# Kernel tuning notes

Measured on AMD Instinct MI355X. Metric: run time of the kernel, lower is better.

The kernel has to match this reference:

```python
import jax, jax.numpy as jnp
import numpy as np

B, C_IN, L = 1024, 3, 2048
D, K = 64, 8192          # embedding_dim, num_embeddings
BETA = 0.25
SLOPE = 0.001            # LeakyReLU negative slope


def _leaky(x):
    return jnp.where(x > 0, x, SLOPE * x)


def setup_inputs() -> dict:
    key = jax.random.key(0)
    ks = jax.random.split(key, 16)
    def lin(k, fan_in, shape):  # torch default conv init ~ U(-1/sqrt(fan_in), 1/sqrt(fan_in))
        b = 1.0 / np.sqrt(fan_in)
        return jax.random.uniform(k, shape, jnp.float32, -b, b)
    inp = {
        "x":  jax.random.normal(ks[0], (B, C_IN, L), jnp.float32),
        # encoder conv1x1 weights stored as [out, in]
        "W1": lin(ks[1], C_IN, (64, C_IN)),  "b1": lin(ks[2], C_IN, (64,)),
        "W2": lin(ks[3], 64,   (128, 64)),   "b2": lin(ks[4], 64,  (128,)),
        "W3": lin(ks[5], 128,  (D, 128)),    "b3": lin(ks[6], 128, (D,)),
        # codebook init: uniform(-1/K, 1/K) as in the torch module
        "codebook": jax.random.uniform(ks[7], (K, D), jnp.float32, -1.0 / K, 1.0 / K),
        # decoder convtranspose1x1 weights stored as [in, out]
        "U1": lin(ks[8],  D,   (D, 128)),    "c1": lin(ks[9],  D,   (128,)),
        "U2": lin(ks[10], 128, (128, 64)),   "c2": lin(ks[11], 128, (64,)),
        "U3": lin(ks[12], 64,  (64, C_IN)),  "c3": lin(ks[13], 64,  (C_IN,)),
    }
    return inp


def reference(x, W1, b1, W2, b2, W3, b3, codebook, U1, c1, U2, c2, U3, c3):
    # ---- encoder: conv1x1 stack over [B, C, L] then global max pool ----
    h = _leaky(jnp.einsum('oc,bcl->bol', W1, x) + b1[None, :, None])   # [B,64,L]
    h = _leaky(jnp.einsum('oc,bcl->bol', W2, h) + b2[None, :, None])   # [B,128,L]
    h = jnp.einsum('oc,bcl->bol', W3, h) + b3[None, :, None]           # [B,D,L]
    z = jnp.max(h, axis=-1)                                            # [B,D]

    # ---- vector quantizer ----
    d = (jnp.sum(z * z, axis=1, keepdims=True)
         + jnp.sum(codebook * codebook, axis=1)
         - 2.0 * z @ codebook.T)                                       # [B,K]
    idx = jnp.argmin(d, axis=1)                                        # [B]
    z_q = codebook[idx]                                                # [B,D]
    sg = jax.lax.stop_gradient
    loss = jnp.mean((sg(z_q) - z) ** 2) + BETA * jnp.mean((z_q - sg(z)) ** 2)
    z_q_st = z + sg(z_q - z)                                           # straight-through

    # ---- decoder: convtranspose1x1 on length-1 sequence == dense layers ----
    g = _leaky(z_q_st @ U1 + c1)                                       # [B,128]
    g = _leaky(g @ U2 + c2)                                            # [B,64]
    x_recon = (g @ U3 + c3)[:, :, None]                                # [B,3,1]
    return x_recon, loss, z
```

## Files before the change

### kernel.cpp

```cpp
#include <hip/hip_runtime.h>
#include <hip/hip_bf16.h>

#define BB 1024
#define LL 2048
#define KK 8192

typedef _Float16 f16x8 __attribute__((ext_vector_type(8)));
typedef _Float16 f16x4 __attribute__((ext_vector_type(4)));
typedef _Float16 f16x2 __attribute__((ext_vector_type(2)));
typedef float    f32x4 __attribute__((ext_vector_type(4)));

__device__ __forceinline__ float leakyf(float v){ return fmaxf(v, 0.001f*v); }
__device__ __forceinline__ f16x2 pkrtz(float a, float b){
    return __builtin_bit_cast(f16x2, __builtin_amdgcn_cvt_pkrtz(a, b));
}
__device__ __forceinline__ f32x4 mfma_w(f16x8 a, f16x8 w_agpr, f32x4 c){
    f32x4 d;
    asm("v_mfma_f32_16x16x32_f16 %0, %1, %2, %3"
        : "=v"(d) : "v"(a), "a"(w_agpr), "v"(c));
    return d;
}

__global__ __launch_bounds__(256, 2) void encoder_mfma(
    const float* __restrict__ x,
    const float* __restrict__ W1, const float* __restrict__ b1,
    const float* __restrict__ W2, const float* __restrict__ b2,
    const float* __restrict__ W3, const float* __restrict__ b3,
    float* __restrict__ z_out, _Float16* __restrict__ zh_out)
{
    const int b    = blockIdx.x;
    const int t    = threadIdx.x;
    const int wave = t >> 6;
    const int lane = t & 63;
    const int col  = lane & 15;
    const int quad = lane >> 4;

    __shared__ __align__(16) _Float16 h2lds[4*16*136];
    __shared__ float red[4][64];

    f16x8 w2f[2][8];
    #pragma unroll
    for (int ks=0; ks<2; ks++){
        #pragma unroll
        for (int nt=0; nt<8; nt++){
            const float* p = W2 + (nt*16+col)*64 + quad*8 + 32*ks;
            f16x8 f;
            #pragma unroll
            for (int j=0;j<8;j++) f[j] = (_Float16)p[j];
            w2f[ks][nt] = f;
        }
    }
    f16x8 w3f[4][4];
    #pragma unroll
    for (int ks=0; ks<4; ks++){
        #pragma unroll
        for (int nt=0; nt<4; nt++){
            const float* p = W3 + (nt*16+col)*128 + quad*8 + 32*ks;
            f16x8 f;
            #pragma unroll
            for (int j=0;j<8;j++) f[j] = (_Float16)p[j];
            w3f[ks][nt] = f;
        }
    }
    f16x2 w1p[2][4][3];
    f16x2 b1p[2][4];
    #pragma unroll
    for (int ks=0; ks<2; ks++){
        #pragma unroll
        for (int j2=0; j2<4; j2++){
            int c0 = quad*8 + 2*j2 + 32*ks;
            #pragma unroll
            for (int i=0;i<3;i++){
                f16x2 w; w[0] = (_Float16)W1[c0*3+i]; w[1] = (_Float16)W1[(c0+1)*3+i];
                w1p[ks][j2][i] = w;
            }
            f16x2 bb; bb[0] = (_Float16)b1[c0]; bb[1] = (_Float16)b1[c0+1];
            b1p[ks][j2] = bb;
        }
    }
    f16x2 b2p[8];
    #pragma unroll
    for (int nt=0; nt<8; nt++){
        _Float16 bv = (_Float16)b2[nt*16+col];
        f16x2 p; p[0]=bv; p[1]=bv; b2p[nt]=p;
    }

    f16x2 k001; k001[0] = (_Float16)0.001f; k001[1] = (_Float16)0.001f;
    f32x4 zc; zc[0]=0.f; zc[1]=0.f; zc[2]=0.f; zc[3]=0.f;

    f32x4 hm[4];
    #pragma unroll
    for (int nt=0;nt<4;nt++){
        hm[nt][0] = -__builtin_inff(); hm[nt][1] = -__builtin_inff();
        hm[nt][2] = -__builtin_inff(); hm[nt][3] = -__builtin_inff();
    }

    const float* xb = x + (size_t)b*3*LL;
    const int wave_off = wave*2176;
    const int pbase = wave*16 + col;
    const int rswz  = (col >> 2) << 4;

    float x0n = xb[pbase], x1n = xb[LL+pbase], x2n = xb[2*LL+pbase];

    #pragma unroll 1
    for (int it=0; it<LL/64; it++){
        const float x0 = x0n, x1 = x1n, x2 = x2n;
        {
            int itn = it+1 < 32 ? it+1 : 31;
            int pn = itn*64 + pbase;
            x0n = xb[pn]; x1n = xb[LL+pn]; x2n = xb[2*LL+pn];
        }
        f16x2 xh0; xh0[0] = (_Float16)x0; xh0[1] = xh0[0];
        f16x2 xh1; xh1[0] = (_Float16)x1; xh1[1] = xh1[0];
        f16x2 xh2; xh2[0] = (_Float16)x2; xh2[1] = xh2[0];

        f16x8 a2[2];
        #pragma unroll
        for (int ks=0; ks<2; ks++){
            f16x8 a;
            #pragma unroll
            for (int j2=0; j2<4; j2++){
                f16x2 v = b1p[ks][j2];
                v += w1p[ks][j2][0]*xh0;
                v += w1p[ks][j2][1]*xh1;
                v += w1p[ks][j2][2]*xh2;
                v = __builtin_elementwise_max(v, v*k001);
                a[2*j2]   = v[0];
                a[2*j2+1] = v[1];
            }
            a2[ks] = a;
        }

        #pragma unroll
        for (int nt=0; nt<8; nt++){
            f32x4 acc = mfma_w(a2[0], w2f[0][nt], zc);
            acc = mfma_w(a2[1], w2f[1][nt], acc);
            f16x2 p01 = pkrtz(acc[0], acc[1]);
            f16x2 p23 = pkrtz(acc[2], acc[3]);
            p01 += b2p[nt];  p23 += b2p[nt];
            p01 = __builtin_elementwise_max(p01, p01*k001);
            p23 = __builtin_elementwise_max(p23, p23*k001);
            _Float16* wp = &h2lds[wave_off + quad*4*136 + ((nt ^ quad)<<4) + col];
            wp[0]     = p01[0];
            wp[136]   = p01[1];
            wp[272]   = p23[0];
            wp[408]   = p23[1];
        }

        f16x8 a30 = *(const f16x8*)&h2lds[wave_off + col*136 + (( 0 + quad*8) ^ rswz)];
        f16x8 a31 = *(const f16x8*)&h2lds[wave_off + col*136 + ((32 + quad*8) ^ rswz)];
        f16x8 a32 = *(const f16x8*)&h2lds[wave_off + col*136 + ((64 + quad*8) ^ rswz)];
        f16x8 a33 = *(const f16x8*)&h2lds[wave_off + col*136 + ((96 + quad*8) ^ rswz)];
        #pragma unroll
        for (int nt=0; nt<4; nt++){
            f32x4 acc = mfma_w(a30, w3f[0][nt], zc);
            acc = mfma_w(a31, w3f[1][nt], acc);
            acc = mfma_w(a32, w3f[2][nt], acc);
            acc = mfma_w(a33, w3f[3][nt], acc);
            hm[nt][0] = fmaxf(hm[nt][0], acc[0]);
            hm[nt][1] = fmaxf(hm[nt][1], acc[1]);
            hm[nt][2] = fmaxf(hm[nt][2], acc[2]);
            hm[nt][3] = fmaxf(hm[nt][3], acc[3]);
        }
    }

    #pragma unroll
    for (int nt=0; nt<4; nt++){
        float v = fmaxf(fmaxf(hm[nt][0], hm[nt][1]), fmaxf(hm[nt][2], hm[nt][3]));
        v = fmaxf(v, __shfl_xor(v, 16, 64));
        v = fmaxf(v, __shfl_xor(v, 32, 64));
        if (quad == 0) red[wave][nt*16 + col] = v;
    }
    __syncthreads();
    if (t < 64){
        float v = fmaxf(fmaxf(red[0][t], red[1][t]), fmaxf(red[2][t], red[3][t])) + b3[t];
        z_out[(size_t)b*64 + t] = v;
        zh_out[(size_t)b*64 + t] = (_Float16)v;
    }
}

__global__ __launch_bounds__(256, 2) void vq_mfma(
    const _Float16* __restrict__ zh, const float* __restrict__ cb,
    float* __restrict__ pval, int* __restrict__ pidx)
{
    const int t    = threadIdx.x;
    const int wave = t >> 6;
    const int lane = t & 63;
    const int col  = lane & 15;
    const int quad = lane >> 4;
    const int rb   = blockIdx.x >> 5;
    const int ns   = blockIdx.x & 31;

    __shared__ __align__(16) _Float16 cbl[256*72];
    __shared__ float cnl[256];

    const int eoff = wave*4 + (lane >> 4);
    const int sub  = lane & 15;
    #pragma unroll 4
    for (int p=0; p<16; p++){
        const int el = p*16 + eoff;
        const float4 v = *(const float4*)(cb + ((size_t)(ns*256 + el))*64 + sub*4);
        f16x2 h0 = pkrtz(v.x, v.y);
        f16x2 h1 = pkrtz(v.z, v.w);
        f16x4 hv; hv[0]=h0[0]; hv[1]=h0[1]; hv[2]=h1[0]; hv[3]=h1[1];
        *(f16x4*)(cbl + el*72 + sub*4) = hv;
        float d = v.x*v.x + v.y*v.y + v.z*v.z + v.w*v.w;
        #pragma unroll
        for (int s=1; s<16; s<<=1) d += __shfl_xor(d, s, 64);
        if (sub == 0) cnl[el] = d;
    }
    __syncthreads();

    const int rowbase = rb*64 + wave*16;
    f16x8 az[2];
    az[0] = *(const f16x8*)&zh[(size_t)(rowbase+col)*64 + quad*8];
    az[1] = *(const f16x8*)&zh[(size_t)(rowbase+col)*64 + quad*8 + 32];

    f32x4 zc; zc[0]=0.f; zc[1]=0.f; zc[2]=0.f; zc[3]=0.f;
    float best[4] = {__builtin_inff(),__builtin_inff(),__builtin_inff(),__builtin_inff()};
    int   bidx[4] = {0,0,0,0};

    #pragma unroll 4
    for (int nt=0; nt<16; nt++){
        const int el = nt*16 + col;
        f16x8 c0 = *(const f16x8*)&cbl[el*72 + quad*8];
        f16x8 c1 = *(const f16x8*)&cbl[el*72 + quad*8 + 32];
        float cnc = cnl[el];
        f32x4 acc = __builtin_amdgcn_mfma_f32_16x16x32_f16(az[0], c0, zc, 0,0,0);
        acc = __builtin_amdgcn_mfma_f32_16x16x32_f16(az[1], c1, acc, 0,0,0);
        const int myidx = ns*256 + el;
        #pragma unroll
        for (int r=0; r<4; r++){
            float d = fmaf(-2.0f, acc[r], cnc);
            if (d < best[r]){ best[r] = d; bidx[r] = myidx; }
        }
    }

    #pragma unroll
    for (int r=0; r<4; r++){
        float v = best[r]; int i = bidx[r];
        #pragma unroll
        for (int s=1; s<16; s<<=1){
            float ov = __shfl_xor(v, s, 64);
            int   oi = __shfl_xor(i, s, 64);
            if (ov < v || (ov == v && oi < i)){ v = ov; i = oi; }
        }
        if (col == 0){
            int row = rowbase + quad*4 + r;
            pval[row*32 + ns] = v;
            pidx[row*32 + ns] = i;
        }
    }
}

__global__ __launch_bounds__(128, 2) void decoder_kernel(
    const float* __restrict__ z,
    const float* __restrict__ pval, const int* __restrict__ pidx,
    const float* __restrict__ cb,
    const float* __restrict__ U1, const float* __restrict__ c1,
    const float* __restrict__ U2, const float* __restrict__ c2,
    const float* __restrict__ U3, const float* __restrict__ c3,
    float* __restrict__ xrec, float* __restrict__ loss_part)
{
    const int b = blockIdx.x;
    const int t = threadIdx.x;
    __shared__ int kk_s;
    __shared__ float zst[64];
    __shared__ float g1[128];
    __shared__ float g2[64];
    if (t < 32){
        float v = pval[b*32 + t]; int i = pidx[b*32 + t];
        #pragma unroll
        for (int s=1; s<32; s<<=1){
            float ov = __shfl_xor(v, s, 32);
            int   oi = __shfl_xor(i, s, 32);
            if (ov < v || (ov == v && oi < i)){ v = ov; i = oi; }
        }
        if (t==0) kk_s = i;
    }
    __syncthreads();
    const int kk = kk_s;
    if (t < 64){
        float zv = z[(size_t)b*64 + t];
        float zq = cb[(size_t)kk*64 + t];
        float diff = zq - zv;
        zst[t] = zv + diff;
        float p = diff*diff;
        #pragma unroll
        for (int s=32;s>0;s>>=1) p += __shfl_xor(p, s, 64);
        if (t==0) loss_part[b] = p;
    }
    __syncthreads();
    {
        float v = c1[t];
        #pragma unroll
        for (int d=0; d<64; d++) v = fmaf(zst[d], U1[d*128+t], v);
        g1[t] = leakyf(v);
    }
    __syncthreads();
    if (t < 64){
        float v = c2[t];
        #pragma unroll
        for (int j=0;j<128;j++) v = fmaf(g1[j], U2[j*64+t], v);
        g2[t] = leakyf(v);
    }
    __syncthreads();
    if (t < 3){
        float v = c3[t];
        #pragma unroll
        for (int j=0;j<64;j++) v = fmaf(g2[j], U3[j*3+t], v);
        xrec[(size_t)b*3 + t] = v;
    }
}

__global__ __launch_bounds__(256, 1) void loss_kernel(
    const float* __restrict__ loss_part, float* __restrict__ out)
{
    const int t = threadIdx.x;
    float s = 0.f;
    for (int i=t;i<BB;i+=256) s += loss_part[i];
    #pragma unroll
    for (int sh=32;sh>0;sh>>=1) s += __shfl_xor(s, sh, 64);
    __shared__ float w[4];
    if ((t&63)==0) w[t>>6] = s;
    __syncthreads();
    if (t==0) out[0] = (w[0]+w[1]+w[2]+w[3]) * (1.25f / 65536.0f);
}

extern "C" void kernel_launch(void* const* d_in, const int* in_sizes, int n_in,
                              void* d_out, int out_size, void* d_ws, size_t ws_size,
                              hipStream_t stream)
{
    const float* x  = (const float*)d_in[0];
    const float* W1 = (const float*)d_in[1];
    const float* b1 = (const float*)d_in[2];
    const float* W2 = (const float*)d_in[3];
    const float* b2 = (const float*)d_in[4];
    const float* W3 = (const float*)d_in[5];
    const float* b3 = (const float*)d_in[6];
    const float* cb = (const float*)d_in[7];
    const float* U1 = (const float*)d_in[8];
    const float* c1 = (const float*)d_in[9];
    const float* U2 = (const float*)d_in[10];
    const float* c2 = (const float*)d_in[11];
    const float* U3 = (const float*)d_in[12];
    const float* c3 = (const float*)d_in[13];

    float* out  = (float*)d_out;
    float* xrec = out;
    float* loss = out + 3072;
    float* z    = out + 3073;

    char* ws = (char*)d_ws;
    float*    lp    = (float*)ws;
    _Float16* zh    = (_Float16*)(ws + 4096);
    float*    pval  = (float*)(ws + 135168);
    int*      pidx  = (int*)(ws + 266240);

    hipLaunchKernelGGL(encoder_mfma, dim3(BB), dim3(256), 0, stream,
                       x, W1, b1, W2, b2, W3, b3, z, zh);
    hipLaunchKernelGGL(vq_mfma, dim3(512), dim3(256), 0, stream, zh, cb, pval, pidx);
    hipLaunchKernelGGL(decoder_kernel, dim3(BB), dim3(128), 0, stream,
                       z, pval, pidx, cb, U1, c1, U2, c2, U3, c3, xrec, lp);
    hipLaunchKernelGGL(loss_kernel, dim3(1), dim3(256), 0, stream, lp, loss);
}
```

Baseline: 211.4 us.

## Pack LDS writes via DPP swaps and precompute codebook norms in separate kernel

In the encoder, the 16-bit scalar stores of layer-2 activations into LDS are replaced by 32-bit stores. Neighbouring lanes exchange halves with a DPP quad-permute and v_perm, so each lane writes two packed fp16 values, halving the number of LDS store instructions in the hot loop. Separately, the codebook squared norms are computed once by a new small kernel instead of by shuffle reductions in every VQ block. The VQ kernel now reads those norms from global memory. This adds one kernel launch and a global read per tile in exchange for removing the redundant reductions.

```diff
diff --git a/kernel.cpp b/kernel.cpp
--- a/kernel.cpp
+++ b/kernel.cpp
@@ -35,8 +35,9 @@
     const int col  = lane & 15;
     const int quad = lane >> 4;
 
-    __shared__ __align__(16) _Float16 h2lds[4*16*136];
+    __shared__ __align__(16) unsigned h2l[4*16*68];
     __shared__ float red[4][64];
+    _Float16* h2h = (_Float16*)h2l;
 
     f16x8 w2f[2][8];
     #pragma unroll
@@ -96,9 +97,10 @@
     }
 
     const float* xb = x + (size_t)b*3*LL;
-    const int wave_off = wave*2176;
     const int pbase = wave*16 + col;
     const int rswz  = (col >> 2) << 4;
+    const int wbase = wave*1088 + (quad*4 + (col&1))*68 + (col>>1);
+    const unsigned selA = (col & 1) ? 0x03020706u : 0x05040100u;
 
     float x0n = xb[pbase], x1n = xb[LL+pbase], x2n = xb[2*LL+pbase];
 
@@ -140,17 +142,22 @@
             p01 += b2p[nt];  p23 += b2p[nt];
             p01 = __builtin_elementwise_max(p01, p01*k001);
             p23 = __builtin_elementwise_max(p23, p23*k001);
-            _Float16* wp = &h2lds[wave_off + quad*4*136 + ((nt ^ quad)<<4) + col];
-            wp[0]     = p01[0];
-            wp[136]   = p01[1];
-            wp[272]   = p23[0];
-            wp[408]   = p23[1];
-        }
-
-        f16x8 a30 = *(const f16x8*)&h2lds[wave_off + col*136 + (( 0 + quad*8) ^ rswz)];
-        f16x8 a31 = *(const f16x8*)&h2lds[wave_off + col*136 + ((32 + quad*8) ^ rswz)];
-        f16x8 a32 = *(const f16x8*)&h2lds[wave_off + col*136 + ((64 + quad*8) ^ rswz)];
-        f16x8 a33 = *(const f16x8*)&h2lds[wave_off + col*136 + ((96 + quad*8) ^ rswz)];
+            unsigned P01 = __builtin_bit_cast(unsigned, p01);
+            unsigned P23 = __builtin_bit_cast(unsigned, p23);
+            unsigned Q01 = (unsigned)__builtin_amdgcn_mov_dpp((int)P01, 0xB1, 0xF, 0xF, true);
+            unsigned Q23 = (unsigned)__builtin_amdgcn_mov_dpp((int)P23, 0xB1, 0xF, 0xF, true);
+            unsigned d0 = __builtin_amdgcn_perm(Q01, P01, selA);
+            unsigned d1 = __builtin_amdgcn_perm(Q23, P23, selA);
+            unsigned* wp = &h2l[wbase + ((nt ^ quad)<<3)];
+            wp[0]   = d0;
+            wp[136] = d1;
+        }
+
+        const int roff = wave*2176 + col*136;
+        f16x8 a30 = *(const f16x8*)&h2h[roff + (( 0 + quad*8) ^ rswz)];
+        f16x8 a31 = *(const f16x8*)&h2h[roff + ((32 + quad*8) ^ rswz)];
+        f16x8 a32 = *(const f16x8*)&h2h[roff + ((64 + quad*8) ^ rswz)];
+        f16x8 a33 = *(const f16x8*)&h2h[roff + ((96 + quad*8) ^ rswz)];
         #pragma unroll
         for (int nt=0; nt<4; nt++){
             f32x4 acc = mfma_w(a30, w3f[0][nt], zc);
@@ -179,8 +186,23 @@
     }
 }
 
+__global__ __launch_bounds__(256, 4) void cnorm_kernel(
+    const float* __restrict__ cb, float* __restrict__ cnorm)
+{
+    const int e = blockIdx.x*256 + threadIdx.x;
+    const float4* p = (const float4*)(cb + (size_t)e*64);
+    float s = 0.f;
+    #pragma unroll
+    for (int q=0;q<16;q++){
+        float4 v = p[q];
+        s += v.x*v.x + v.y*v.y + v.z*v.z + v.w*v.w;
+    }
+    cnorm[e] = s;
+}
+
 __global__ __launch_bounds__(256, 2) void vq_mfma(
     const _Float16* __restrict__ zh, const float* __restrict__ cb,
+    const float* __restrict__ cnorm,
     float* __restrict__ pval, int* __restrict__ pidx)
 {
     const int t    = threadIdx.x;
@@ -192,7 +214,6 @@
     const int ns   = blockIdx.x & 31;
 
     __shared__ __align__(16) _Float16 cbl[256*72];
-    __shared__ float cnl[256];
 
     const int eoff = wave*4 + (lane >> 4);
     const int sub  = lane & 15;
@@ -204,10 +225,6 @@
         f16x2 h1 = pkrtz(v.z, v.w);
         f16x4 hv; hv[0]=h0[0]; hv[1]=h0[1]; hv[2]=h1[0]; hv[3]=h1[1];
         *(f16x4*)(cbl + el*72 + sub*4) = hv;
-        float d = v.x*v.x + v.y*v.y + v.z*v.z + v.w*v.w;
-        #pragma unroll
-        for (int s=1; s<16; s<<=1) d += __shfl_xor(d, s, 64);
-        if (sub == 0) cnl[el] = d;
     }
     __syncthreads();
 
@@ -225,7 +242,7 @@
         const int el = nt*16 + col;
         f16x8 c0 = *(const f16x8*)&cbl[el*72 + quad*8];
         f16x8 c1 = *(const f16x8*)&cbl[el*72 + quad*8 + 32];
-        float cnc = cnl[el];
+        float cnc = cnorm[ns*256 + el];
         f32x4 acc = __builtin_amdgcn_mfma_f32_16x16x32_f16(az[0], c0, zc, 0,0,0);
         acc = __builtin_amdgcn_mfma_f32_16x16x32_f16(az[1], c1, acc, 0,0,0);
         const int myidx = ns*256 + el;
@@ -356,10 +373,12 @@
     _Float16* zh    = (_Float16*)(ws + 4096);
     float*    pval  = (float*)(ws + 135168);
     int*      pidx  = (int*)(ws + 266240);
-
+    float*    cnorm = (float*)(ws + 397312);
+
+    hipLaunchKernelGGL(cnorm_kernel, dim3(KK/256), dim3(256), 0, stream, cb, cnorm);
     hipLaunchKernelGGL(encoder_mfma, dim3(BB), dim3(256), 0, stream,
                        x, W1, b1, W2, b2, W3, b3, z, zh);
-    hipLaunchKernelGGL(vq_mfma, dim3(512), dim3(256), 0, stream, zh, cb, pval, pidx);
+    hipLaunchKernelGGL(vq_mfma, dim3(512), dim3(256), 0, stream, zh, cb, cnorm, pval, pidx);
     hipLaunchKernelGGL(decoder_kernel, dim3(BB), dim3(128), 0, stream,
                        z, pval, pidx, cb, U1, c1, U2, c2, U3, c3, xrec, lp);
     hipLaunchKernelGGL(loss_kernel, dim3(1), dim3(256), 0, stream, lp, loss);
```

Measured after the change: 206.4 us. 1.02x faster.
